# Kernel optimization log

Measured on AMD Instinct MI355X. Metric: run time of the kernel, lower is better.

Reference implementation:

```python
import jax, jax.numpy as jnp
import numpy as np

N_ATOMS = 50000
N_EDGES = 640000
D = 128
N_RBF = 20
N_INTER = 3

act = jax.nn.softplus


def setup_inputs() -> dict:
    key = jax.random.key(0)
    ks = jax.random.split(key, 16)
    s = 1.0 / np.sqrt(D)
    inp = {
        "x": jax.random.normal(ks[0], (N_ATOMS, D), jnp.float32),
        "g_ij": jax.random.uniform(ks[1], (N_EDGES, N_RBF), jnp.float32),
        "idx_i": jax.random.randint(ks[2], (N_EDGES,), 0, N_ATOMS),
        "idx_j": jax.random.randint(ks[3], (N_EDGES,), 0, N_ATOMS),
        "n_atoms": N_ATOMS,
        "u": jnp.ones((D,), jnp.float32),
        "Wf": jax.random.normal(ks[4], (D, D), jnp.float32) * s,
        "bf": jnp.zeros((D,), jnp.float32),
        # linear_g weight init to zero in original; use small random so grads flow
        "Wg": jax.random.normal(ks[5], (D, N_RBF), jnp.float32) * 0.01,
        "bg": jnp.zeros((D,), jnp.float32),
        "Wj": jax.random.normal(ks[6], (D, D), jnp.float32) * s,
        "bj": jnp.zeros((D,), jnp.float32),
        "Wi": jax.random.normal(ks[7], (D, D), jnp.float32) * s,
        "bi": jnp.zeros((D,), jnp.float32),
        "res_w1": jax.random.normal(ks[8], (N_INTER, D, D), jnp.float32) * s,
        "res_b1": jnp.zeros((N_INTER, D), jnp.float32),
        "res_w2": jax.random.normal(ks[9], (N_INTER, D, D), jnp.float32) * s,
        "res_b2": jnp.zeros((N_INTER, D), jnp.float32),
    }
    return inp


def reference(x, g_ij, idx_i, idx_j, n_atoms, u, Wf, bf, Wg, bg, Wj, bj, Wi, bi,
              res_w1, res_b1, res_w2, res_b2):
    x_j = x[idx_j]                                    # [E, D] gather
    xp = u * x                                        # [N, D]
    # sequential_j: act -> linear_j -> act, gated by linear_g(g_ij)
    vp = act(act(x_j) @ Wj.T + bj) * (g_ij @ Wg.T + bg)   # [E, D]
    vm = act(act(x) @ Wi.T + bi)                      # [N, D]
    v = jax.ops.segment_sum(vp, idx_i, num_segments=n_atoms) + vm
    for l in range(res_w1.shape[0]):
        h = act(v) @ res_w1[l].T + res_b1[l]
        h = act(h) @ res_w2[l].T + res_b2[l]
        v = h + v
    v = act(v)
    return xp + v @ Wf.T + bf
```

## Files before the change

### kernel.cpp

```cpp
#include <hip/hip_runtime.h>
#include <hip/hip_fp16.h>

#define DD 128

typedef __attribute__((ext_vector_type(8))) short short8;
typedef __attribute__((ext_vector_type(8))) unsigned short ushort8;
typedef __attribute__((ext_vector_type(4))) float floatx4;
typedef unsigned int uint32;

__device__ __forceinline__ float sp(float x) {
    return fmaxf(x, 0.0f) + __logf(1.0f + __expf(-fabsf(x)));
}

__device__ __forceinline__ unsigned short f2bf(float f) {
    union { float f; uint32 u; } c; c.f = f;
    const uint32 u = c.u;
    return (unsigned short)((u + 0x7fffu + ((u >> 16) & 1u)) >> 16);
}

__device__ __forceinline__ unsigned short f2h(float f) {
    __half h = __float2half(f);
    return __builtin_bit_cast(unsigned short, h);
}

__global__ __launch_bounds__(256)
void convert_w(const float* __restrict__ Wj, const float* __restrict__ Wi,
               const float* __restrict__ rw1, const float* __restrict__ rw2,
               const float* __restrict__ Wf, unsigned short* __restrict__ out,
               const float* __restrict__ g, unsigned short* __restrict__ gh,
               int gchunks)
{
    if ((int)blockIdx.x >= 72) {
        const int gid = ((int)blockIdx.x - 72) * 256 + threadIdx.x;
        if (gid < gchunks) {
            const float4 f0 = reinterpret_cast<const float4*>(g)[2 * gid];
            const float4 f1 = reinterpret_cast<const float4*>(g)[2 * gid + 1];
            ushort8 o;
            o[0] = f2h(f0.x); o[1] = f2h(f0.y); o[2] = f2h(f0.z); o[3] = f2h(f0.w);
            o[4] = f2h(f1.x); o[5] = f2h(f1.y); o[6] = f2h(f1.z); o[7] = f2h(f1.w);
            reinterpret_cast<ushort8*>(gh)[gid] = o;
        }
        return;
    }
    const int gid = blockIdx.x * 256 + threadIdx.x;
    const int mat = gid >> 11;
    const int f8  = gid & 2047;
    const float* src;
    if      (mat == 0) src = Wj;
    else if (mat == 1) src = Wi;
    else if (mat <= 4) src = rw1 + (size_t)(mat - 2) * 16384;
    else if (mat <= 7) src = rw2 + (size_t)(mat - 5) * 16384;
    else               src = Wf;
    const int row = f8 >> 4;
    const int ch  = f8 & 15;
    const float4 a = reinterpret_cast<const float4*>(src)[2 * f8];
    const float4 b = reinterpret_cast<const float4*>(src)[2 * f8 + 1];
    ushort8 u8;
    u8[0] = f2bf(a.x); u8[1] = f2bf(a.y); u8[2] = f2bf(a.z); u8[3] = f2bf(a.w);
    u8[4] = f2bf(b.x); u8[5] = f2bf(b.y); u8[6] = f2bf(b.z); u8[7] = f2bf(b.w);
    *reinterpret_cast<ushort8*>(out + (size_t)mat * 16384 + row * 128 +
                                ((ch ^ (row & 15)) << 3)) = u8;
}

__device__ __forceinline__ void stage_wb(const unsigned short* __restrict__ Wb,
                                         unsigned short* wl, int t)
{
    #pragma unroll
    for (int i = 0; i < 8; ++i) {
        const int c = t + i * 256;
        *reinterpret_cast<ushort8*>(wl + c * 8) =
            *reinterpret_cast<const ushort8*>(Wb + c * 8);
    }
}

__device__ __forceinline__ void load_afrag_act(const float* __restrict__ X,
                                               int m, int q, int n, short8 af[4])
{
    const int mm = m < n ? m : n - 1;
    const float* row = X + (size_t)mm * DD + q * 8;
    #pragma unroll
    for (int kk = 0; kk < 4; ++kk) {
        const float4 a = *reinterpret_cast<const float4*>(row + kk * 32);
        const float4 b = *reinterpret_cast<const float4*>(row + kk * 32 + 4);
        ushort8 u;
        u[0] = f2bf(sp(a.x)); u[1] = f2bf(sp(a.y)); u[2] = f2bf(sp(a.z)); u[3] = f2bf(sp(a.w));
        u[4] = f2bf(sp(b.x)); u[5] = f2bf(sp(b.y)); u[6] = f2bf(sp(b.z)); u[7] = f2bf(sp(b.w));
        af[kk] = __builtin_bit_cast(short8, u);
    }
}

__device__ __forceinline__ void mfma_gemm(const unsigned short* wl,
                                          const short8 af[4],
                                          int cl, int q, floatx4 acc[8])
{
    #pragma unroll
    for (int nt = 0; nt < 8; ++nt) {
        const int nrow = nt * 16 + cl;
        #pragma unroll
        for (int kk = 0; kk < 4; ++kk) {
            const int chs = (kk * 4 + q) ^ cl;
            const short8 bfr = *reinterpret_cast<const short8*>(wl + nrow * 128 + (chs << 3));
            acc[nt] = __builtin_amdgcn_mfma_f32_16x16x32_bf16(af[kk], bfr, acc[nt], 0, 0, 0);
        }
    }
}

__global__ __launch_bounds__(256, 4)
void dual_gemm(const float* __restrict__ x,
               const unsigned short* __restrict__ Wb,
               const float* __restrict__ bj, const float* __restrict__ bi,
               unsigned short* __restrict__ Aout, float* __restrict__ vout, int n)
{
    __shared__ __align__(16) unsigned short wl[128 * 128];
    const int t = threadIdx.x;
    const int lane = t & 63, wv = t >> 6;
    const int cl = lane & 15, q = lane >> 4;
    const int m0 = blockIdx.x * 64 + wv * 16;

    short8 af[4];
    load_afrag_act(x, m0 + cl, q, n, af);

    stage_wb(Wb, wl, t);
    __syncthreads();

    floatx4 acc[8];
    #pragma unroll
    for (int nt = 0; nt < 8; ++nt) acc[nt] = (floatx4){0.f, 0.f, 0.f, 0.f};
    mfma_gemm(wl, af, cl, q, acc);

    #pragma unroll
    for (int nt = 0; nt < 8; ++nt) {
        const int col = nt * 16 + cl;
        const float bb = bj[col];
        #pragma unroll
        for (int r = 0; r < 4; ++r) {
            const int row = m0 + q * 4 + r;
            if (row < n) Aout[(size_t)row * DD + col] = f2bf(sp(acc[nt][r] + bb));
        }
    }

    __syncthreads();
    stage_wb(Wb + 16384, wl, t);
    __syncthreads();

    #pragma unroll
    for (int nt = 0; nt < 8; ++nt) acc[nt] = (floatx4){0.f, 0.f, 0.f, 0.f};
    mfma_gemm(wl, af, cl, q, acc);

    #pragma unroll
    for (int nt = 0; nt < 8; ++nt) {
        const int col = nt * 16 + cl;
        const float bb = bi[col];
        #pragma unroll
        for (int r = 0; r < 4; ++r) {
            const int row = m0 + q * 4 + r;
            if (row < n) vout[(size_t)row * DD + col] = sp(acc[nt][r] + bb);
        }
    }
}

__global__ __launch_bounds__(256, 2)
void tail_kernel(const float* __restrict__ vin, const float* __restrict__ x,
                 const unsigned short* __restrict__ Wb,
                 const float* __restrict__ rb1, const float* __restrict__ rb2,
                 const float* __restrict__ bf, const float* __restrict__ u,
                 float* __restrict__ out, int n)
{
    __shared__ __align__(16) unsigned short wl[128 * 128];
    __shared__ __align__(16) unsigned short hl[64 * 128];
    __shared__ __align__(16) float vt[64 * 128];
    const int t = threadIdx.x;
    const int lane = t & 63, wv = t >> 6;
    const int cl = lane & 15, q = lane >> 4;
    const int mb = blockIdx.x * 64;

    #pragma unroll
    for (int i = 0; i < 8; ++i) {
        const int c = t + i * 256;
        const int row = c >> 5;
        const int chv = c & 31;
        float4 val = make_float4(0.f, 0.f, 0.f, 0.f);
        if (mb + row < n) val = reinterpret_cast<const float4*>(vin)[(size_t)mb * 32 + c];
        *reinterpret_cast<float4*>(vt + row * 128 + ((chv ^ (row & 15)) << 2)) = val;
    }
    stage_wb(Wb + 2 * 16384, wl, t);
    __syncthreads();

    floatx4 vac[8];
    #pragma unroll
    for (int nt = 0; nt < 8; ++nt) {
        #pragma unroll
        for (int r = 0; r < 4; ++r) {
            const int rl = wv * 16 + q * 4 + r;
            const int col = nt * 16 + cl;
            const int chv = col >> 2;
            vac[nt][r] = vt[rl * 128 + ((chv ^ (rl & 15)) << 2) + (col & 3)];
        }
    }

    short8 af[4];
    {
        const int rl = wv * 16 + cl;
        #pragma unroll
        for (int kk = 0; kk < 4; ++kk) {
            const int c0 = q * 2 + kk * 8;
            const floatx4 A0 = *reinterpret_cast<const floatx4*>(vt + rl * 128 + (((c0    ) ^ cl) << 2));
            const floatx4 A1 = *reinterpret_cast<const floatx4*>(vt + rl * 128 + (((c0 + 1) ^ cl) << 2));
            ushort8 u8;
            u8[0] = f2bf(sp(A0[0])); u8[1] = f2bf(sp(A0[1])); u8[2] = f2bf(sp(A0[2])); u8[3] = f2bf(sp(A0[3]));
            u8[4] = f2bf(sp(A1[0])); u8[5] = f2bf(sp(A1[1])); u8[6] = f2bf(sp(A1[2])); u8[7] = f2bf(sp(A1[3]));
            af[kk] = __builtin_bit_cast(short8, u8);
        }
    }

    const int ml2 = wv * 16 + cl;

    for (int l = 0; l < 3; ++l) {
        if (l > 0) {
            #pragma unroll
            for (int nt = 0; nt < 8; ++nt) {
                const int col = nt * 16 + cl;
                const int ch = col >> 3;
                #pragma unroll
                for (int r = 0; r < 4; ++r) {
                    const int ml = wv * 16 + q * 4 + r;
                    hl[ml * 128 + ((ch ^ (ml & 15)) << 3) + (col & 7)] = f2bf(sp(vac[nt][r]));
                }
            }
            #pragma unroll
            for (int kk = 0; kk < 4; ++kk)
                af[kk] = *reinterpret_cast<const short8*>(hl + ml2 * 128 + (((kk * 4 + q) ^ cl) << 3));
            __syncthreads();
            stage_wb(Wb + (size_t)(2 + l) * 16384, wl, t);
            __syncthreads();
        }

        floatx4 acc[8];
        #pragma unroll
        for (int nt = 0; nt < 8; ++nt) acc[nt] = (floatx4){0.f, 0.f, 0.f, 0.f};
        mfma_gemm(wl, af, cl, q, acc);

        const float* b1 = rb1 + (size_t)l * DD;
        #pragma unroll
        for (int nt = 0; nt < 8; ++nt) {
            const int col = nt * 16 + cl;
            const int ch = col >> 3;
            const float bb = b1[col];
            #pragma unroll
            for (int r = 0; r < 4; ++r) {
                const int ml = wv * 16 + q * 4 + r;
                hl[ml * 128 + ((ch ^ (ml & 15)) << 3) + (col & 7)] = f2bf(sp(acc[nt][r] + bb));
            }
        }
        short8 af2[4];
        #pragma unroll
        for (int kk = 0; kk < 4; ++kk)
            af2[kk] = *reinterpret_cast<const short8*>(hl + ml2 * 128 + (((kk * 4 + q) ^ cl) << 3));

        __syncthreads();
        stage_wb(Wb + (size_t)(5 + l) * 16384, wl, t);
        __syncthreads();

        #pragma unroll
        for (int nt = 0; nt < 8; ++nt) acc[nt] = (floatx4){0.f, 0.f, 0.f, 0.f};
        mfma_gemm(wl, af2, cl, q, acc);

        const float* b2 = rb2 + (size_t)l * DD;
        #pragma unroll
        for (int nt = 0; nt < 8; ++nt) {
            const float bb = b2[nt * 16 + cl];
            #pragma unroll
            for (int r = 0; r < 4; ++r) vac[nt][r] += acc[nt][r] + bb;
        }
    }

    __syncthreads();
    stage_wb(Wb + (size_t)8 * 16384, wl, t);
    #pragma unroll
    for (int i = 0; i < 8; ++i) {
        const int c = t + i * 256;
        const int row = c >> 5;
        const int chv = c & 31;
        float4 val = make_float4(0.f, 0.f, 0.f, 0.f);
        if (mb + row < n) val = reinterpret_cast<const float4*>(x)[(size_t)mb * 32 + c];
        *reinterpret_cast<float4*>(vt + row * 128 + ((chv ^ (row & 15)) << 2)) = val;
    }
    __syncthreads();

    #pragma unroll
    for (int nt = 0; nt < 8; ++nt) {
        const int col = nt * 16 + cl;
        const int ch = col >> 3;
        #pragma unroll
        for (int r = 0; r < 4; ++r) {
            const int ml = wv * 16 + q * 4 + r;
            hl[ml * 128 + ((ch ^ (ml & 15)) << 3) + (col & 7)] = f2bf(sp(vac[nt][r]));
        }
    }
    short8 aff[4];
    #pragma unroll
    for (int kk = 0; kk < 4; ++kk)
        aff[kk] = *reinterpret_cast<const short8*>(hl + ml2 * 128 + (((kk * 4 + q) ^ cl) << 3));

    floatx4 acc[8];
    #pragma unroll
    for (int nt = 0; nt < 8; ++nt) acc[nt] = (floatx4){0.f, 0.f, 0.f, 0.f};
    mfma_gemm(wl, aff, cl, q, acc);

    #pragma unroll
    for (int nt = 0; nt < 8; ++nt) {
        const int col = nt * 16 + cl;
        const float bb = bf[col];
        const float uu = u[col];
        const int chv = col >> 2;
        #pragma unroll
        for (int r = 0; r < 4; ++r) {
            const int rl = wv * 16 + q * 4 + r;
            const int row = mb + rl;
            if (row < n) {
                const float xv = vt[rl * 128 + ((chv ^ (rl & 15)) << 2) + (col & 3)];
                out[(size_t)row * DD + col] = acc[nt][r] + bb + uu * xv;
            }
        }
    }
}


__global__ __launch_bounds__(256)
void hist_kernel(const int* __restrict__ idx_i, int* __restrict__ cnt, int E)
{
    const int e = blockIdx.x * 256 + threadIdx.x;
    if (e < E) atomicAdd(&cnt[idx_i[e]], 1);
}

__global__ __launch_bounds__(256)
void scan_reduce(const int* __restrict__ cnt, int* __restrict__ bsum, int n)
{
    __shared__ int wsum[4];
    const int t = threadIdx.x;
    const int lane = t & 63, wv = t >> 6;
    const int i0 = blockIdx.x * 1024 + t * 4;
    int s = 0;
    #pragma unroll
    for (int k = 0; k < 4; ++k) if (i0 + k < n) s += cnt[i0 + k];
    #pragma unroll
    for (int d = 1; d < 64; d <<= 1) s += __shfl_down(s, d, 64);
    if (lane == 0) wsum[wv] = s;
    __syncthreads();
    if (t == 0) bsum[blockIdx.x] = wsum[0] + wsum[1] + wsum[2] + wsum[3];
}

__global__ __launch_bounds__(256)
void scan_apply(const int* __restrict__ cnt, const int* __restrict__ bsum,
                int* __restrict__ off, int* __restrict__ cnt2, int n, int nb)
{
    __shared__ int wsum[4];
    const int t = threadIdx.x;
    const int lane = t & 63, wv = t >> 6;

    int bval = (lane < nb && lane < (int)blockIdx.x) ? bsum[lane] : 0;
    #pragma unroll
    for (int d = 32; d >= 1; d >>= 1) bval += __shfl_down(bval, d, 64);
    const int blk_off = __shfl(bval, 0, 64);

    const int i0 = blockIdx.x * 1024 + t * 4;
    const int v0 = (i0 + 0 < n) ? cnt[i0 + 0] : 0;
    const int v1 = (i0 + 1 < n) ? cnt[i0 + 1] : 0;
    const int v2 = (i0 + 2 < n) ? cnt[i0 + 2] : 0;
    const int v3 = (i0 + 3 < n) ? cnt[i0 + 3] : 0;
    const int s = v0 + v1 + v2 + v3;
    int incl = s;
    #pragma unroll
    for (int d = 1; d < 64; d <<= 1) {
        const int y = __shfl_up(incl, d, 64);
        if (lane >= d) incl += y;
    }
    if (lane == 63) wsum[wv] = incl;
    __syncthreads();
    int woff = blk_off;
    #pragma unroll
    for (int w = 0; w < 4; ++w) if (w < wv) woff += wsum[w];
    const int excl = woff + incl - s;
    if (i0 + 0 < n) { off[i0 + 0] = excl;                cnt2[i0 + 0] = 0; }
    if (i0 + 1 < n) { off[i0 + 1] = excl + v0;           cnt2[i0 + 1] = 0; }
    if (i0 + 2 < n) { off[i0 + 2] = excl + v0 + v1;      cnt2[i0 + 2] = 0; }
    if (i0 + 3 < n) { off[i0 + 3] = excl + v0 + v1 + v2; cnt2[i0 + 3] = 0; }
}

__global__ __launch_bounds__(256)
void scatter_kernel(const int* __restrict__ idx_i, const int* __restrict__ idx_j,
                    const int* __restrict__ off, int* __restrict__ cnt2,
                    int2* __restrict__ spair, int E)
{
    const int e = blockIdx.x * 256 + threadIdx.x;
    if (e < E) {
        const int i = idx_i[e];
        const int p = off[i] + atomicAdd(&cnt2[i], 1);
        spair[p] = make_int2(e, idx_j[e]);
    }
}

template<int GH>
__global__ __launch_bounds__(256, 4)
void agg_kernel(const int* __restrict__ off, const int* __restrict__ cnt,
                const int2* __restrict__ spair,
                const unsigned short* __restrict__ gh,
                const float* __restrict__ g,
                const float* __restrict__ Wg, const float* __restrict__ bg,
                const unsigned short* __restrict__ A, float* __restrict__ v, int N)
{
    const int t = threadIdx.x;
    const int lane = t & 63;
    const int wid0 = blockIdx.x * 4 + (t >> 6);
    const int nw   = gridDim.x * 4;
    const int d0 = lane << 1;

    const float bg0 = bg[d0], bg1 = bg[d0 + 1];

    if (GH) {
        __half2 w0h[10], w1h[10];
        #pragma unroll
        for (int k2 = 0; k2 < 10; ++k2) {
            w0h[k2] = __floats2half2_rn(Wg[d0 * 20 + 2 * k2], Wg[d0 * 20 + 2 * k2 + 1]);
            w1h[k2] = __floats2half2_rn(Wg[(d0 + 1) * 20 + 2 * k2], Wg[(d0 + 1) * 20 + 2 * k2 + 1]);
        }

        for (int i = wid0; i < N; i += nw) {
            const int beg = off[i], num = cnt[i], end = beg + num;
            float2 acc = *reinterpret_cast<const float2*>(v + (size_t)i * DD + d0);

            int p = beg;
            while (p + 4 <= end) {
                int ee[4], jj[4];
                #pragma unroll
                for (int u = 0; u < 4; ++u) {
                    const int2 pr = spair[p + u];
                    ee[u] = __builtin_amdgcn_readfirstlane(pr.x);
                    jj[u] = __builtin_amdgcn_readfirstlane(pr.y);
                }
                uint32 aa[4];
                float2 gq[4][5];
                #pragma unroll
                for (int u = 0; u < 4; ++u) {
                    aa[u] = *reinterpret_cast<const uint32*>(A + (size_t)jj[u] * DD + d0);
                    const float2* gp = reinterpret_cast<const float2*>(gh + (size_t)ee[u] * 20);
                    #pragma unroll
                    for (int q2 = 0; q2 < 5; ++q2) gq[u][q2] = gp[q2];
                }
                #pragma unroll
                for (int u = 0; u < 4; ++u) {
                    __half2 a0 = __float2half2_rn(0.f), a1 = __float2half2_rn(0.f);
                    #pragma unroll
                    for (int q2 = 0; q2 < 5; ++q2) {
                        const __half2 h0 = __builtin_bit_cast(__half2, gq[u][q2].x);
                        const __half2 h1 = __builtin_bit_cast(__half2, gq[u][q2].y);
                        a0 = __hfma2(h0, w0h[2 * q2], a0);
                        a1 = __hfma2(h0, w1h[2 * q2], a1);
                        a0 = __hfma2(h1, w0h[2 * q2 + 1], a0);
                        a1 = __hfma2(h1, w1h[2 * q2 + 1], a1);
                    }
                    const float t0 = bg0 + __low2float(a0) + __high2float(a0);
                    const float t1 = bg1 + __low2float(a1) + __high2float(a1);
                    union { uint32 u32; float f; } cx, cy;
                    cx.u32 = aa[u] << 16;
                    cy.u32 = aa[u] & 0xffff0000u;
                    acc.x = fmaf(cx.f, t0, acc.x);
                    acc.y = fmaf(cy.f, t1, acc.y);
                }
                p += 4;
            }
            for (; p < end; ++p) {
                const int2 pr = spair[p];
                const int e0 = __builtin_amdgcn_readfirstlane(pr.x);
                const int j0 = __builtin_amdgcn_readfirstlane(pr.y);
                const uint32 a0u = *reinterpret_cast<const uint32*>(A + (size_t)j0 * DD + d0);
                const float2* gp = reinterpret_cast<const float2*>(gh + (size_t)e0 * 20);
                __half2 a0 = __float2half2_rn(0.f), a1 = __float2half2_rn(0.f);
                #pragma unroll
                for (int q2 = 0; q2 < 5; ++q2) {
                    const float2 qq = gp[q2];
                    const __half2 h0 = __builtin_bit_cast(__half2, qq.x);
                    const __half2 h1 = __builtin_bit_cast(__half2, qq.y);
                    a0 = __hfma2(h0, w0h[2 * q2], a0);
                    a1 = __hfma2(h0, w1h[2 * q2], a1);
                    a0 = __hfma2(h1, w0h[2 * q2 + 1], a0);
                    a1 = __hfma2(h1, w1h[2 * q2 + 1], a1);
                }
                const float t0 = bg0 + __low2float(a0) + __high2float(a0);
                const float t1 = bg1 + __low2float(a1) + __high2float(a1);
                union { uint32 u32; float f; } cx, cy;
                cx.u32 = a0u << 16;
                cy.u32 = a0u & 0xffff0000u;
                acc.x = fmaf(cx.f, t0, acc.x);
                acc.y = fmaf(cy.f, t1, acc.y);
            }
            *reinterpret_cast<float2*>(v + (size_t)i * DD + d0) = acc;
        }
    } else {
        float2 wg01[20];
        #pragma unroll
        for (int k = 0; k < 20; ++k) {
            wg01[k].x = Wg[d0 * 20 + k];
            wg01[k].y = Wg[(d0 + 1) * 20 + k];
        }
        for (int i = wid0; i < N; i += nw) {
            const int beg = off[i], num = cnt[i], end = beg + num;
            float2 acc = *reinterpret_cast<const float2*>(v + (size_t)i * DD + d0);
            int p = beg;
            for (; p + 2 <= end; p += 2) {
                const int2 pr0 = spair[p];
                const int2 pr1 = spair[p + 1];
                const int e0 = __builtin_amdgcn_readfirstlane(pr0.x);
                const int j0 = __builtin_amdgcn_readfirstlane(pr0.y);
                const int e1 = __builtin_amdgcn_readfirstlane(pr1.x);
                const int j1 = __builtin_amdgcn_readfirstlane(pr1.y);
                const uint32 a0 = *reinterpret_cast<const uint32*>(A + (size_t)j0 * DD + d0);
                const uint32 a1 = *reinterpret_cast<const uint32*>(A + (size_t)j1 * DD + d0);
                const float4* g0p = reinterpret_cast<const float4*>(g + (size_t)e0 * 20);
                const float4* g1p = reinterpret_cast<const float4*>(g + (size_t)e1 * 20);
                float2 t0 = make_float2(bg0, bg1), t1 = make_float2(bg0, bg1);
                #pragma unroll
                for (int qq = 0; qq < 5; ++qq) {
                    const float4 p0 = g0p[qq];
                    const float4 p1 = g1p[qq];
                    t0.x = fmaf(p0.x, wg01[qq*4+0].x, t0.x); t0.y = fmaf(p0.x, wg01[qq*4+0].y, t0.y);
                    t0.x = fmaf(p0.y, wg01[qq*4+1].x, t0.x); t0.y = fmaf(p0.y, wg01[qq*4+1].y, t0.y);
                    t0.x = fmaf(p0.z, wg01[qq*4+2].x, t0.x); t0.y = fmaf(p0.z, wg01[qq*4+2].y, t0.y);
                    t0.x = fmaf(p0.w, wg01[qq*4+3].x, t0.x); t0.y = fmaf(p0.w, wg01[qq*4+3].y, t0.y);
                    t1.x = fmaf(p1.x, wg01[qq*4+0].x, t1.x); t1.y = fmaf(p1.x, wg01[qq*4+0].y, t1.y);
                    t1.x = fmaf(p1.y, wg01[qq*4+1].x, t1.x); t1.y = fmaf(p1.y, wg01[qq*4+1].y, t1.y);
                    t1.x = fmaf(p1.z, wg01[qq*4+2].x, t1.x); t1.y = fmaf(p1.z, wg01[qq*4+2].y, t1.y);
                    t1.x = fmaf(p1.w, wg01[qq*4+3].x, t1.x); t1.y = fmaf(p1.w, wg01[qq*4+3].y, t1.y);
                }
                union { uint32 u; float f; } c0x, c0y, c1x, c1y;
                c0x.u = a0 << 16; c0y.u = a0 & 0xffff0000u;
                c1x.u = a1 << 16; c1y.u = a1 & 0xffff0000u;
                acc.x = fmaf(c0x.f, t0.x, acc.x); acc.y = fmaf(c0y.f, t0.y, acc.y);
                acc.x = fmaf(c1x.f, t1.x, acc.x); acc.y = fmaf(c1y.f, t1.y, acc.y);
            }
            if (p < end) {
                const int2 pr0 = spair[p];
                const int e0 = __builtin_amdgcn_readfirstlane(pr0.x);
                const int j0 = __builtin_amdgcn_readfirstlane(pr0.y);
                const uint32 a0 = *reinterpret_cast<const uint32*>(A + (size_t)j0 * DD + d0);
                const float4* g0p = reinterpret_cast<const float4*>(g + (size_t)e0 * 20);
                float2 t0 = make_float2(bg0, bg1);
                #pragma unroll
                for (int qq = 0; qq < 5; ++qq) {
                    const float4 p0 = g0p[qq];
                    t0.x = fmaf(p0.x, wg01[qq*4+0].x, t0.x); t0.y = fmaf(p0.x, wg01[qq*4+0].y, t0.y);
                    t0.x = fmaf(p0.y, wg01[qq*4+1].x, t0.x); t0.y = fmaf(p0.y, wg01[qq*4+1].y, t0.y);
                    t0.x = fmaf(p0.z, wg01[qq*4+2].x, t0.x); t0.y = fmaf(p0.z, wg01[qq*4+2].y, t0.y);
                    t0.x = fmaf(p0.w, wg01[qq*4+3].x, t0.x); t0.y = fmaf(p0.w, wg01[qq*4+3].y, t0.y);
                }
                union { uint32 u; float f; } c0x, c0y;
                c0x.u = a0 << 16; c0y.u = a0 & 0xffff0000u;
                acc.x = fmaf(c0x.f, t0.x, acc.x); acc.y = fmaf(c0y.f, t0.y, acc.y);
            }
            *reinterpret_cast<float2*>(v + (size_t)i * DD + d0) = acc;
        }
    }
}

extern "C" void kernel_launch(void* const* d_in, const int* in_sizes, int n_in,
                              void* d_out, int out_size, void* d_ws, size_t ws_size,
                              hipStream_t stream)
{
    const float* x     = (const float*)d_in[0];
    const float* g     = (const float*)d_in[1];
    const int*   idx_i = (const int*)d_in[2];
    const int*   idx_j = (const int*)d_in[3];
    const float* u     = (const float*)d_in[5];
    const float* Wf    = (const float*)d_in[6];
    const float* bf    = (const float*)d_in[7];
    const float* Wg    = (const float*)d_in[8];
    const float* bg    = (const float*)d_in[9];
    const float* Wj    = (const float*)d_in[10];
    const float* bj    = (const float*)d_in[11];
    const float* Wi    = (const float*)d_in[12];
    const float* bi    = (const float*)d_in[13];
    const float* rw1   = (const float*)d_in[14];
    const float* rb1   = (const float*)d_in[15];
    const float* rw2   = (const float*)d_in[16];
    const float* rb2   = (const float*)d_in[17];

    const int N = in_sizes[0] / DD;
    const int E = in_sizes[2];
    float* out = (float*)d_out;

    float*          v     = (float*)d_ws;
    unsigned short* A     = (unsigned short*)(v + (size_t)N * DD);
    int*            cnt   = (int*)(A + (size_t)N * DD);
    int*            off   = cnt + N;
    int*            cnt2  = off + N;
    int*            bsum  = cnt2 + N;
    int2*           spair = (int2*)(bsum + 64);
    unsigned short* Wb    = (unsigned short*)(spair + E);
    unsigned short* gh    = Wb + 9 * 16384;

    const size_t need_gh = (size_t)((char*)(gh + (size_t)E * 20) - (char*)d_ws);
    const bool gh_ok = ws_size >= need_gh;

    dim3 blk(256);
    const int tiles    = (N + 63) / 64;
    const int eblocks  = (E + 255) / 256;
    const int sblocks  = (N + 1023) / 1024;
    const int gchunks  = gh_ok ? (E * 20) / 8 : 0;
    const int gblocks  = gh_ok ? (gchunks + 255) / 256 : 0;

    convert_w<<<72 + gblocks, blk, 0, stream>>>(Wj, Wi, rw1, rw2, Wf, Wb,
                                                g, gh, gchunks);

    hipMemsetAsync(cnt, 0, (size_t)N * sizeof(int), stream);
    hist_kernel<<<eblocks, blk, 0, stream>>>(idx_i, cnt, E);
    scan_reduce<<<sblocks, blk, 0, stream>>>(cnt, bsum, N);
    scan_apply<<<sblocks, blk, 0, stream>>>(cnt, bsum, off, cnt2, N, sblocks);
    scatter_kernel<<<eblocks, blk, 0, stream>>>(idx_i, idx_j, off, cnt2, spair, E);

    dual_gemm<<<tiles, blk, 0, stream>>>(x, Wb, bj, bi, A, v, N);

    if (gh_ok)
        agg_kernel<1><<<2048, blk, 0, stream>>>(off, cnt, spair, gh, g,
                                                Wg, bg, A, v, N);
    else
        agg_kernel<0><<<2048, blk, 0, stream>>>(off, cnt, spair, gh, g,
                                                Wg, bg, A, v, N);

    tail_kernel<<<tiles, blk, 0, stream>>>(v, x, Wb, rb1, rb2, bf, u, out, N);
}
```

Baseline: 242.7 us.

## Drop vt shared buffer and register-prefetch next weight matrix in tail kernel

Removes the 32KB fp32 vt shared tile from tail_kernel, loading residual values and activation fragments straight from global memory and reading x directly in the epilogue. Each next weight matrix is now prefetched into registers while the current MFMA runs, so the global load overlaps compute instead of stalling between syncs. The second GEMM accumulates directly into vac. The smaller LDS footprint allows raising launch bounds to 3 blocks per CU. The costs are more register pressure from the wreg buffer and uncoalesced strided global loads for vin and x.

```diff
diff --git a/kernel.cpp b/kernel.cpp
--- a/kernel.cpp
+++ b/kernel.cpp
@@ -159,7 +159,7 @@
     }
 }
 
-__global__ __launch_bounds__(256, 2)
+__global__ __launch_bounds__(256, 3)
 void tail_kernel(const float* __restrict__ vin, const float* __restrict__ x,
                  const unsigned short* __restrict__ Wb,
                  const float* __restrict__ rb1, const float* __restrict__ rb2,
@@ -168,53 +168,32 @@
 {
     __shared__ __align__(16) unsigned short wl[128 * 128];
     __shared__ __align__(16) unsigned short hl[64 * 128];
-    __shared__ __align__(16) float vt[64 * 128];
     const int t = threadIdx.x;
     const int lane = t & 63, wv = t >> 6;
     const int cl = lane & 15, q = lane >> 4;
     const int mb = blockIdx.x * 64;
-
-    #pragma unroll
-    for (int i = 0; i < 8; ++i) {
-        const int c = t + i * 256;
-        const int row = c >> 5;
-        const int chv = c & 31;
-        float4 val = make_float4(0.f, 0.f, 0.f, 0.f);
-        if (mb + row < n) val = reinterpret_cast<const float4*>(vin)[(size_t)mb * 32 + c];
-        *reinterpret_cast<float4*>(vt + row * 128 + ((chv ^ (row & 15)) << 2)) = val;
-    }
+    const int ml2 = wv * 16 + cl;
+
+    floatx4 vac[8];
+    #pragma unroll
+    for (int nt = 0; nt < 8; ++nt) {
+        #pragma unroll
+        for (int r = 0; r < 4; ++r) {
+            const int row = mb + wv * 16 + q * 4 + r;
+            const int col = nt * 16 + cl;
+            vac[nt][r] = (row < n) ? vin[(size_t)row * DD + col] : 0.f;
+        }
+    }
+
+    short8 af[4];
+    load_afrag_act(vin, mb + wv * 16 + cl, q, n, af);
+
     stage_wb(Wb + 2 * 16384, wl, t);
     __syncthreads();
 
-    floatx4 vac[8];
-    #pragma unroll
-    for (int nt = 0; nt < 8; ++nt) {
-        #pragma unroll
-        for (int r = 0; r < 4; ++r) {
-            const int rl = wv * 16 + q * 4 + r;
-            const int col = nt * 16 + cl;
-            const int chv = col >> 2;
-            vac[nt][r] = vt[rl * 128 + ((chv ^ (rl & 15)) << 2) + (col & 3)];
-        }
-    }
-
-    short8 af[4];
-    {
-        const int rl = wv * 16 + cl;
-        #pragma unroll
-        for (int kk = 0; kk < 4; ++kk) {
-            const int c0 = q * 2 + kk * 8;
-            const floatx4 A0 = *reinterpret_cast<const floatx4*>(vt + rl * 128 + (((c0    ) ^ cl) << 2));
-            const floatx4 A1 = *reinterpret_cast<const floatx4*>(vt + rl * 128 + (((c0 + 1) ^ cl) << 2));
-            ushort8 u8;
-            u8[0] = f2bf(sp(A0[0])); u8[1] = f2bf(sp(A0[1])); u8[2] = f2bf(sp(A0[2])); u8[3] = f2bf(sp(A0[3]));
-            u8[4] = f2bf(sp(A1[0])); u8[5] = f2bf(sp(A1[1])); u8[6] = f2bf(sp(A1[2])); u8[7] = f2bf(sp(A1[3]));
-            af[kk] = __builtin_bit_cast(short8, u8);
-        }
-    }
-
-    const int ml2 = wv * 16 + cl;
-
+    ushort8 wreg[8];
+
+    #pragma unroll
     for (int l = 0; l < 3; ++l) {
         if (l > 0) {
             #pragma unroll
@@ -230,10 +209,11 @@
             #pragma unroll
             for (int kk = 0; kk < 4; ++kk)
                 af[kk] = *reinterpret_cast<const short8*>(hl + ml2 * 128 + (((kk * 4 + q) ^ cl) << 3));
-            __syncthreads();
-            stage_wb(Wb + (size_t)(2 + l) * 16384, wl, t);
-            __syncthreads();
-        }
+        }
+
+        #pragma unroll
+        for (int i = 0; i < 8; ++i)
+            wreg[i] = *reinterpret_cast<const ushort8*>(Wb + (size_t)(5 + l) * 16384 + (t + i * 256) * 8);
 
         floatx4 acc[8];
         #pragma unroll
@@ -258,34 +238,31 @@
             af2[kk] = *reinterpret_cast<const short8*>(hl + ml2 * 128 + (((kk * 4 + q) ^ cl) << 3));
 
         __syncthreads();
-        stage_wb(Wb + (size_t)(5 + l) * 16384, wl, t);
+        #pragma unroll
+        for (int i = 0; i < 8; ++i)
+            *reinterpret_cast<ushort8*>(wl + (t + i * 256) * 8) = wreg[i];
         __syncthreads();
 
-        #pragma unroll
-        for (int nt = 0; nt < 8; ++nt) acc[nt] = (floatx4){0.f, 0.f, 0.f, 0.f};
-        mfma_gemm(wl, af2, cl, q, acc);
-
+        const int nxt = (l < 2) ? (3 + l) : 8;
+        #pragma unroll
+        for (int i = 0; i < 8; ++i)
+            wreg[i] = *reinterpret_cast<const ushort8*>(Wb + (size_t)nxt * 16384 + (t + i * 256) * 8);
+
+        mfma_gemm(wl, af2, cl, q, vac);
         const float* b2 = rb2 + (size_t)l * DD;
         #pragma unroll
         for (int nt = 0; nt < 8; ++nt) {
             const float bb = b2[nt * 16 + cl];
             #pragma unroll
-            for (int r = 0; r < 4; ++r) vac[nt][r] += acc[nt][r] + bb;
-        }
-    }
-
-    __syncthreads();
-    stage_wb(Wb + (size_t)8 * 16384, wl, t);
-    #pragma unroll
-    for (int i = 0; i < 8; ++i) {
-        const int c = t + i * 256;
-        const int row = c >> 5;
-        const int chv = c & 31;
-        float4 val = make_float4(0.f, 0.f, 0.f, 0.f);
-        if (mb + row < n) val = reinterpret_cast<const float4*>(x)[(size_t)mb * 32 + c];
-        *reinterpret_cast<float4*>(vt + row * 128 + ((chv ^ (row & 15)) << 2)) = val;
-    }
-    __syncthreads();
+            for (int r = 0; r < 4; ++r) vac[nt][r] += bb;
+        }
+
+        __syncthreads();
+        #pragma unroll
+        for (int i = 0; i < 8; ++i)
+            *reinterpret_cast<ushort8*>(wl + (t + i * 256) * 8) = wreg[i];
+        __syncthreads();
+    }
 
     #pragma unroll
     for (int nt = 0; nt < 8; ++nt) {
@@ -312,15 +289,12 @@
         const int col = nt * 16 + cl;
         const float bb = bf[col];
         const float uu = u[col];
-        const int chv = col >> 2;
         #pragma unroll
         for (int r = 0; r < 4; ++r) {
-            const int rl = wv * 16 + q * 4 + r;
-            const int row = mb + rl;
-            if (row < n) {
-                const float xv = vt[rl * 128 + ((chv ^ (rl & 15)) << 2) + (col & 3)];
-                out[(size_t)row * DD + col] = acc[nt][r] + bb + uu * xv;
-            }
+            const int row = mb + wv * 16 + q * 4 + r;
+            if (row < n)
+                out[(size_t)row * DD + col] =
+                    acc[nt][r] + bb + uu * x[(size_t)row * DD + col];
         }
     }
 }
```

Result: slower. 253.2 us (+4.3%).
